# Optimization experiments

Measured on AMD Instinct MI355X. Metric: run time of the kernel, lower is better.

## Reference

```python
import jax, jax.numpy as jnp
import numpy as np

LN_EPS = 1e-3  # keras LayerNormalization default epsilon
H = 32


def _glorot(key, shape):
    fan_in, fan_out = shape[0], shape[1]
    lim = np.sqrt(6.0 / (fan_in + fan_out)).astype(np.float32)
    return jax.random.uniform(key, shape, jnp.float32, -lim, lim)


def setup_inputs() -> dict:
    key = jax.random.key(0)
    ks = jax.random.split(key, 10)
    ns, nc, d = 4096, 1024, 64
    num_seq, seq_len = 32, 256
    return {
        "sites": jax.random.normal(ks[0], (ns, d), jnp.float32),
        "cons": jax.random.normal(ks[1], (nc, d), jnp.float32),
        "idx_lower": jax.random.randint(ks[2], (ns,), 0, num_seq * seq_len, jnp.int32),
        "idx_higher": jax.random.randint(ks[3], (ns,), 0, num_seq * seq_len, jnp.int32),
        "W_s": _glorot(ks[4], (d, H)), "b_s": jnp.zeros((H,), jnp.float32),
        "W_c": _glorot(ks[5], (d, H)), "b_c": jnp.zeros((H,), jnp.float32),
        "W_d": _glorot(ks[6], (H, H)), "b_d": jnp.zeros((H,), jnp.float32),
        "ln_g": jnp.ones((H,), jnp.float32), "ln_b": jnp.zeros((H,), jnp.float32),
        "W_o": _glorot(ks[7], (H, 1)), "b_o": jnp.zeros((1,), jnp.float32),
        "num_seq": num_seq, "seq_len": seq_len,
    }


def reference(sites, cons, idx_lower, idx_higher, W_s, b_s, W_c, b_c,
              W_d, b_d, ln_g, ln_b, W_o, b_o, num_seq, seq_len):
    s = jax.nn.relu(sites @ W_s + b_s)          # [ns, 32]
    c = jax.nn.relu(cons @ W_c + b_c)           # [nc, 32]
    comb = s[:, None, :] + c[None, :, :]        # [ns, nc, 32] broadcast-sum
    h = comb @ W_d + b_d                        # decoder MLP: Dense(32)
    mu = jnp.mean(h, axis=-1, keepdims=True)
    var = jnp.var(h, axis=-1, keepdims=True)
    h = (h - mu) * jax.lax.rsqrt(var + LN_EPS) * ln_g + ln_b  # LayerNorm
    logits = (h @ W_o + b_o)[..., 0]            # [ns, nc]
    M = jax.nn.softmax(logits, axis=-1)

    nc_ = M.shape[1]
    slots = num_seq * seq_len

    def band(cum, idx):
        # scatter_nd (duplicate indices accumulate) onto slot grid
        Z = jnp.zeros((slots, nc_), M.dtype).at[idx].add(cum)
        Z = Z.reshape(num_seq, seq_len, nc_)
        p = jax.nn.relu(1.0 - Z)
        # exclusive cumprod along the position (seq_len) axis
        excl = jnp.cumprod(
            jnp.concatenate([jnp.ones_like(p[:, :1]), p[:, :-1]], axis=1), axis=1)
        return excl.reshape(slots, nc_)[idx]    # gather back per site

    M_c_lower = jnp.flip(jnp.cumsum(jnp.flip(M, -1), axis=-1), -1)  # reverse cumsum
    M_c_higher = jnp.cumsum(M, axis=-1)
    M_lower = band(M_c_lower, idx_lower)
    M_higher = band(M_c_higher, idx_higher)
    return M * M_lower * M_higher
```

## Files before the change

kernel.cpp:

```cpp
#include <hip/hip_runtime.h>

#define NS 4096
#define NCC 1024
#define DD 64
#define HH2 32
#define NSEQ 32
#define SLEN 256
#define SLOTS 8192
#define LNEPS 1e-3f
#define MAXSPS 1024

__global__ void __launch_bounds__(1024) k_setup(
    const float* __restrict__ sites, const float* __restrict__ cons,
    const float* __restrict__ Ws, const float* __restrict__ bs,
    const float* __restrict__ Wc, const float* __restrict__ bc,
    const float* __restrict__ Wd, const float* __restrict__ bd,
    const float* __restrict__ g, const float* __restrict__ Wo,
    float* __restrict__ u, float* __restrict__ A, float* __restrict__ P,
    float* __restrict__ v, float* __restrict__ B, float* __restrict__ Q,
    const int* __restrict__ idxl, const int* __restrict__ idxh,
    int* __restrict__ offl, int* __restrict__ slotl, int* __restrict__ sitel,
    int* __restrict__ offh, int* __restrict__ sloth, int* __restrict__ siteh) {
  __shared__ int cnt[SLOTS];
  __shared__ int wsumI[16];
  int tid = threadIdx.x;
  if (blockIdx.x < 5) {
    int t = blockIdx.x * 1024 + tid;
    if (t >= NS + NCC) return;
    bool isSite = t < NS;
    int row = isSite ? t : t - NS;
    const float* x = isSite ? sites + row * DD : cons + row * DD;
    const float* W1 = isSite ? Ws : Wc;
    const float* b1 = isSite ? bs : bc;
    float s[HH2];
#pragma unroll
    for (int h = 0; h < HH2; h++) s[h] = b1[h];
    for (int k = 0; k < DD; k++) {
      float xv = x[k];
#pragma unroll
      for (int h = 0; h < HH2; h++) s[h] = fmaf(xv, W1[k * HH2 + h], s[h]);
    }
#pragma unroll
    for (int h = 0; h < HH2; h++) s[h] = fmaxf(s[h], 0.0f);
    float hs[HH2];
#pragma unroll
    for (int h = 0; h < HH2; h++) hs[h] = isSite ? 0.0f : bd[h];
    for (int k = 0; k < HH2; k++) {
      float sv = s[k];
#pragma unroll
      for (int h = 0; h < HH2; h++) hs[h] = fmaf(sv, Wd[k * HH2 + h], hs[h]);
    }
    float mu = 0.f;
#pragma unroll
    for (int h = 0; h < HH2; h++) mu += hs[h];
    mu *= (1.0f / HH2);
    float p = 0.f, a = 0.f;
    float* dst = isSite ? (u + row * HH2) : (v + row * HH2);
#pragma unroll
    for (int h = 0; h < HH2; h++) {
      float uu = hs[h] - mu;
      dst[h] = uu;
      p += uu * uu;
      a = fmaf(uu * g[h], Wo[h], a);
    }
    p *= (1.0f / HH2);
    if (isSite) { A[row] = a; P[row] = p; } else { B[row] = a; Q[row] = p; }
    return;
  }
  int lane = tid & 63, wv = tid >> 6;
  int pass = blockIdx.x - 5;
  const int* idx = pass ? idxh : idxl;
  int* off = pass ? offh : offl;
  int* slotA = pass ? sloth : slotl;
  int* siteA = pass ? siteh : sitel;
  for (int i2 = tid; i2 < SLOTS; i2 += 1024) cnt[i2] = 0;
  __syncthreads();
  for (int i2 = tid; i2 < NS; i2 += 1024) atomicAdd(&cnt[idx[i2]], 1);
  __syncthreads();
  int base = tid * 8;
  int loc[8]; int sum = 0;
#pragma unroll
  for (int q2 = 0; q2 < 8; q2++) { loc[q2] = sum; sum += cnt[base + q2]; }
  int incl = sum;
#pragma unroll
  for (int o = 1; o < 64; o <<= 1) { int t2 = __shfl_up(incl, o); if (lane >= o) incl += t2; }
  if (lane == 63) wsumI[wv] = incl;
  __syncthreads();
  int wprev = 0;
#pragma unroll
  for (int w = 0; w < 16; w++) { int t3 = wsumI[w]; if (w < wv) wprev += t3; }
  int excl = wprev + (incl - sum);
  __syncthreads();
#pragma unroll
  for (int q2 = 0; q2 < 8; q2++) { int o2 = excl + loc[q2]; off[base + q2] = o2; cnt[base + q2] = o2; }
  if (tid == 0) off[SLOTS] = NS;
  __syncthreads();
  for (int i2 = tid; i2 < NS; i2 += 1024) {
    int sl = idx[i2];
    int pos = atomicAdd(&cnt[sl], 1);
    slotA[pos] = sl; siteA[pos] = i2;
  }
}

__global__ void __launch_bounds__(1024) k_main(const float* __restrict__ u,
    const float* __restrict__ A, const float* __restrict__ P,
    const float* __restrict__ v, const float* __restrict__ B, const float* __restrict__ Q,
    const float* __restrict__ lnb, const float* __restrict__ Wo, const float* __restrict__ bo,
    float* __restrict__ M, float* __restrict__ CLp, float* __restrict__ CHp) {
  int j = threadIdx.x;
  int lane = j & 63, wv = j >> 6;
  __shared__ float redA[16 * 16];
  __shared__ float redB[16 * 16];
  float4 vv[8];
  const float4* vp = (const float4*)(v + j * HH2);
#pragma unroll
  for (int q = 0; q < 8; q++) vv[q] = vp[q];
  float Bj = B[j], Qj = Q[j];
  float C = bo[0];
#pragma unroll
  for (int k = 0; k < HH2; k++) C = fmaf(lnb[k], Wo[k], C);
  int row0 = blockIdx.x * 16;

  float logit[16];
#pragma unroll
  for (int rr = 0; rr < 16; rr++) {
    int i = row0 + rr;
    const float4* up = (const float4*)(u + i * HH2);
    float dot = 0.f;
#pragma unroll
    for (int q = 0; q < 8; q++) {
      float4 u4 = up[q];
      dot = fmaf(u4.x, vv[q].x, dot);
      dot = fmaf(u4.y, vv[q].y, dot);
      dot = fmaf(u4.z, vv[q].z, dot);
      dot = fmaf(u4.w, vv[q].w, dot);
    }
    float var = P[i] + Qj + dot * 0.0625f;
    float lg = rsqrtf(var + LNEPS) * (A[i] + Bj) + C;
    logit[rr] = lg;
    float mx = lg;
#pragma unroll
    for (int o = 32; o > 0; o >>= 1) mx = fmaxf(mx, __shfl_xor(mx, o));
    if (lane == 0) redA[rr * 16 + wv] = mx;
  }
  __syncthreads();
  float e[16], incl[16];
#pragma unroll
  for (int rr = 0; rr < 16; rr++) {
    const float4* ra = (const float4*)(redA + rr * 16);
    float4 a0 = ra[0], a1 = ra[1], a2 = ra[2], a3 = ra[3];
    float mx = fmaxf(fmaxf(fmaxf(a0.x, a0.y), fmaxf(a0.z, a0.w)),
                     fmaxf(fmaxf(a1.x, a1.y), fmaxf(a1.z, a1.w)));
    mx = fmaxf(mx, fmaxf(fmaxf(fmaxf(a2.x, a2.y), fmaxf(a2.z, a2.w)),
                         fmaxf(fmaxf(a3.x, a3.y), fmaxf(a3.z, a3.w))));
    float ee = __expf(logit[rr] - mx);
    float ic = ee;
#pragma unroll
    for (int o = 1; o < 64; o <<= 1) { float tt = __shfl_up(ic, o); if (lane >= o) ic += tt; }
    if (lane == 63) redB[rr * 16 + wv] = ic;
    e[rr] = ee; incl[rr] = ic;
  }
  __syncthreads();
#pragma unroll
  for (int rr = 0; rr < 16; rr++) {
    const float4* rb = (const float4*)(redB + rr * 16);
    float4 b0 = rb[0], b1 = rb[1], b2 = rb[2], b3 = rb[3];
    float w_[16] = {b0.x, b0.y, b0.z, b0.w, b1.x, b1.y, b1.z, b1.w,
                    b2.x, b2.y, b2.z, b2.w, b3.x, b3.y, b3.z, b3.w};
    float prev = 0.f, tot = 0.f;
#pragma unroll
    for (int w = 0; w < 16; w++) { tot += w_[w]; if (w < wv) prev += w_[w]; }
    float chE = prev + incl[rr];
    float rd = 1.0f / tot;
    int o_ = (row0 + rr) * NCC + j;
    M[o_] = e[rr] * rd;
    CHp[o_] = chE * rd;
    CLp[o_] = (tot - chE + e[rr]) * rd;
  }
}

__global__ void __launch_bounds__(64, 1) k_band(const float* __restrict__ CLp, const float* __restrict__ CHp,
    const int* __restrict__ offl, const int* __restrict__ slotl, const int* __restrict__ sitel,
    const int* __restrict__ offh, const int* __restrict__ sloth, const int* __restrict__ siteh,
    float* __restrict__ EL, float* __restrict__ EH) {
  int band = blockIdx.z;
  const float* cum = band ? CHp : CLp;
  const int* off   = band ? offh : offl;
  const int* slotA = band ? sloth : slotl;
  const int* siteA = band ? siteh : sitel;
  float* E = band ? EH : EL;
  int seq = blockIdx.y;
  int j0 = blockIdx.x * 256 + threadIdx.x * 4;
  int s0 = off[seq * SLEN];
  int s1 = off[seq * SLEN + SLEN];
  int n = s1 - s0;

  __shared__ int s_site[MAXSPS];
  __shared__ int s_slot[MAXSPS];
  for (int i = threadIdx.x; i < n; i += 64) {
    s_site[i] = siteA[s0 + i];
    s_slot[i] = slotA[s0 + i];
  }
  __syncthreads();
  if (n <= 0) return;

  const int T = 8;
  float4 bufA[T], bufB[T];
#pragma unroll
  for (int k = 0; k < T; k++) {
    int kk = k < n ? k : n - 1;
    bufA[k] = *(const float4*)(cum + (size_t)s_site[kk] * NCC + j0);
  }
#pragma unroll
  for (int k = 0; k < T; k++) {
    int kk = T + k < n ? T + k : n - 1;
    bufB[k] = *(const float4*)(cum + (size_t)s_site[kk] * NCC + j0);
  }

  float4 r = make_float4(1.f, 1.f, 1.f, 1.f);
  float4 z = make_float4(0.f, 0.f, 0.f, 0.f);
  int prev = -1;
  int ntiles = (n + T - 1) / T;
  for (int t = 0; t < ntiles; t += 2) {
#pragma unroll
    for (int k = 0; k < T; k++) {
      int cur = t * T + k;
      if (cur < n) {
        float4 cv = bufA[k];
        int slot = s_slot[cur];
        if (slot != prev) {
          if (prev >= 0) {
            r.x *= fmaxf(1.f - z.x, 0.f);
            r.y *= fmaxf(1.f - z.y, 0.f);
            r.z *= fmaxf(1.f - z.z, 0.f);
            r.w *= fmaxf(1.f - z.w, 0.f);
            z = make_float4(0.f, 0.f, 0.f, 0.f);
          }
          prev = slot;
        }
        *(float4*)(E + (size_t)s_site[cur] * NCC + j0) = r;
        z.x += cv.x; z.y += cv.y; z.z += cv.z; z.w += cv.w;
      }
    }
#pragma unroll
    for (int k = 0; k < T; k++) {
      int idx2 = (t + 2) * T + k;
      int kk = idx2 < n ? idx2 : n - 1;
      bufA[k] = *(const float4*)(cum + (size_t)s_site[kk] * NCC + j0);
    }
#pragma unroll
    for (int k = 0; k < T; k++) {
      int cur = (t + 1) * T + k;
      if (cur < n) {
        float4 cv = bufB[k];
        int slot = s_slot[cur];
        if (slot != prev) {
          if (prev >= 0) {
            r.x *= fmaxf(1.f - z.x, 0.f);
            r.y *= fmaxf(1.f - z.y, 0.f);
            r.z *= fmaxf(1.f - z.z, 0.f);
            r.w *= fmaxf(1.f - z.w, 0.f);
            z = make_float4(0.f, 0.f, 0.f, 0.f);
          }
          prev = slot;
        }
        *(float4*)(E + (size_t)s_site[cur] * NCC + j0) = r;
        z.x += cv.x; z.y += cv.y; z.z += cv.z; z.w += cv.w;
      }
    }
#pragma unroll
    for (int k = 0; k < T; k++) {
      int idx2 = (t + 3) * T + k;
      int kk = idx2 < n ? idx2 : n - 1;
      bufB[k] = *(const float4*)(cum + (size_t)s_site[kk] * NCC + j0);
    }
  }
}

__global__ void k_final(float* __restrict__ out, const float* __restrict__ EL,
                        const float* __restrict__ EH) {
  int t = blockIdx.x * blockDim.x + threadIdx.x;
  float4 m = ((const float4*)out)[t];
  float4 a = ((const float4*)EL)[t];
  float4 b = ((const float4*)EH)[t];
  m.x *= a.x * b.x; m.y *= a.y * b.y; m.z *= a.z * b.z; m.w *= a.w * b.w;
  ((float4*)out)[t] = m;
}

extern "C" void kernel_launch(void* const* d_in, const int* in_sizes, int n_in,
                              void* d_out, int out_size, void* d_ws, size_t ws_size,
                              hipStream_t stream) {
  const float* sites = (const float*)d_in[0];
  const float* cons  = (const float*)d_in[1];
  const int* idxl = (const int*)d_in[2];
  const int* idxh = (const int*)d_in[3];
  const float* Ws = (const float*)d_in[4];
  const float* bs = (const float*)d_in[5];
  const float* Wc = (const float*)d_in[6];
  const float* bc = (const float*)d_in[7];
  const float* Wd = (const float*)d_in[8];
  const float* bd = (const float*)d_in[9];
  const float* lng = (const float*)d_in[10];
  const float* lnb = (const float*)d_in[11];
  const float* Wo = (const float*)d_in[12];
  const float* bo = (const float*)d_in[13];

  char* wsb = (char*)d_ws;
  size_t o = 0;
  auto alloc = [&](size_t bytes) { char* p = wsb + o; o += (bytes + 15) & ~(size_t)15; return p; };
  float* u   = (float*)alloc((size_t)NS * HH2 * 4);
  float* A   = (float*)alloc((size_t)NS * 4);
  float* P   = (float*)alloc((size_t)NS * 4);
  float* v   = (float*)alloc((size_t)NCC * HH2 * 4);
  float* B   = (float*)alloc((size_t)NCC * 4);
  float* Q   = (float*)alloc((size_t)NCC * 4);
  float* CLp = (float*)alloc((size_t)NS * NCC * 4);
  float* CHp = (float*)alloc((size_t)NS * NCC * 4);
  float* EL  = (float*)alloc((size_t)NS * NCC * 4);
  float* EH  = (float*)alloc((size_t)NS * NCC * 4);
  int* offl  = (int*)alloc((SLOTS + 1) * 4);
  int* slotl = (int*)alloc(NS * 4);
  int* sitel = (int*)alloc(NS * 4);
  int* offh  = (int*)alloc((SLOTS + 1) * 4);
  int* sloth = (int*)alloc(NS * 4);
  int* siteh = (int*)alloc(NS * 4);

  k_setup<<<7, 1024, 0, stream>>>(sites, cons, Ws, bs, Wc, bc, Wd, bd, lng, Wo,
                                  u, A, P, v, B, Q,
                                  idxl, idxh, offl, slotl, sitel, offh, sloth, siteh);
  k_main<<<NS / 16, 1024, 0, stream>>>(u, A, P, v, B, Q, lnb, Wo, bo,
                                       (float*)d_out, CLp, CHp);
  k_band<<<dim3(4, NSEQ, 2), 64, 0, stream>>>(CLp, CHp, offl, slotl, sitel,
                                              offh, sloth, siteh, EL, EH);
  k_final<<<(NS * NCC / 4) / 256, 256, 0, stream>>>((float*)d_out, EL, EH);
}
```

Before: 182.2 us.

## Fuse all stages into one cooperative persistent kernel with grid syncs

Replaces the four separate launches (setup, main softmax/cumsum, band scan, final multiply) with a single cooperative kernel of 256 blocks that runs each stage in turn, separated by grid-wide syncs. The band stage now gives each 64-lane wave one scalar column strip, mapping 1024 jobs onto 4 waves per block, instead of float4 strips in 64-thread blocks. The setup MLP is spread over 244 blocks of 21 active threads. The aim is to remove launch gaps and to use more of the device in the band stage. In exchange it adds grid-sync overhead, leaves most threads idle during setup, and truncates the per-sequence site count at 512 (MAXSPS cut from 1024), which could give wrong results if that many sites fall in one sequence.

```diff
diff --git a/kernel.cpp b/kernel.cpp
--- a/kernel.cpp
+++ b/kernel.cpp
@@ -1,4 +1,7 @@
 #include <hip/hip_runtime.h>
+#include <hip/hip_cooperative_groups.h>
+
+namespace cg = cooperative_groups;
 
 #define NS 4096
 #define NCC 1024
@@ -8,329 +11,318 @@
 #define SLEN 256
 #define SLOTS 8192
 #define LNEPS 1e-3f
-#define MAXSPS 1024
-
-__global__ void __launch_bounds__(1024) k_setup(
-    const float* __restrict__ sites, const float* __restrict__ cons,
-    const float* __restrict__ Ws, const float* __restrict__ bs,
-    const float* __restrict__ Wc, const float* __restrict__ bc,
-    const float* __restrict__ Wd, const float* __restrict__ bd,
-    const float* __restrict__ g, const float* __restrict__ Wo,
-    float* __restrict__ u, float* __restrict__ A, float* __restrict__ P,
-    float* __restrict__ v, float* __restrict__ B, float* __restrict__ Q,
-    const int* __restrict__ idxl, const int* __restrict__ idxh,
-    int* __restrict__ offl, int* __restrict__ slotl, int* __restrict__ sitel,
-    int* __restrict__ offh, int* __restrict__ sloth, int* __restrict__ siteh) {
-  __shared__ int cnt[SLOTS];
-  __shared__ int wsumI[16];
-  int tid = threadIdx.x;
-  if (blockIdx.x < 5) {
-    int t = blockIdx.x * 1024 + tid;
-    if (t >= NS + NCC) return;
-    bool isSite = t < NS;
-    int row = isSite ? t : t - NS;
-    const float* x = isSite ? sites + row * DD : cons + row * DD;
-    const float* W1 = isSite ? Ws : Wc;
-    const float* b1 = isSite ? bs : bc;
-    float s[HH2];
-#pragma unroll
-    for (int h = 0; h < HH2; h++) s[h] = b1[h];
-    for (int k = 0; k < DD; k++) {
-      float xv = x[k];
-#pragma unroll
-      for (int h = 0; h < HH2; h++) s[h] = fmaf(xv, W1[k * HH2 + h], s[h]);
-    }
-#pragma unroll
-    for (int h = 0; h < HH2; h++) s[h] = fmaxf(s[h], 0.0f);
-    float hs[HH2];
-#pragma unroll
-    for (int h = 0; h < HH2; h++) hs[h] = isSite ? 0.0f : bd[h];
-    for (int k = 0; k < HH2; k++) {
-      float sv = s[k];
-#pragma unroll
-      for (int h = 0; h < HH2; h++) hs[h] = fmaf(sv, Wd[k * HH2 + h], hs[h]);
-    }
-    float mu = 0.f;
-#pragma unroll
-    for (int h = 0; h < HH2; h++) mu += hs[h];
-    mu *= (1.0f / HH2);
-    float p = 0.f, a = 0.f;
-    float* dst = isSite ? (u + row * HH2) : (v + row * HH2);
-#pragma unroll
-    for (int h = 0; h < HH2; h++) {
-      float uu = hs[h] - mu;
-      dst[h] = uu;
-      p += uu * uu;
-      a = fmaf(uu * g[h], Wo[h], a);
-    }
-    p *= (1.0f / HH2);
-    if (isSite) { A[row] = a; P[row] = p; } else { B[row] = a; Q[row] = p; }
-    return;
+#define MAXSPS 512
+
+struct Params {
+  const float *sites, *cons;
+  const int *idxl, *idxh;
+  const float *Ws, *bs, *Wc, *bc, *Wd, *bd, *lng, *lnb, *Wo, *bo;
+  float *out;
+  float *u, *A, *P, *v, *B, *Q, *CL, *CH, *EL, *EH;
+  int *offl, *slotl, *sitel, *offh, *sloth, *siteh;
+};
+
+__global__ void __launch_bounds__(1024, 4) k_all(Params p) {
+  __shared__ union SM {
+    struct { int cnt[SLOTS]; int wsum[16]; } sort;
+    struct { float redA[256]; float redB[256]; } red;
+    struct { int site[4][MAXSPS]; int slot[4][MAXSPS]; } band;
+  } sm;
+  cg::grid_group grid = cg::this_grid();
+  int b = blockIdx.x, tid = threadIdx.x;
+  int lane = tid & 63, wv = tid >> 6;
+
+  if (b < 2) {
+    const int* idx = b ? p.idxh : p.idxl;
+    int* off = b ? p.offh : p.offl;
+    int* slotA = b ? p.sloth : p.slotl;
+    int* siteA = b ? p.siteh : p.sitel;
+    for (int i2 = tid; i2 < SLOTS; i2 += 1024) sm.sort.cnt[i2] = 0;
+    __syncthreads();
+    for (int i2 = tid; i2 < NS; i2 += 1024) atomicAdd(&sm.sort.cnt[idx[i2]], 1);
+    __syncthreads();
+    int base = tid * 8;
+    int loc[8]; int sum = 0;
+#pragma unroll
+    for (int q2 = 0; q2 < 8; q2++) { loc[q2] = sum; sum += sm.sort.cnt[base + q2]; }
+    int incl = sum;
+#pragma unroll
+    for (int o = 1; o < 64; o <<= 1) { int t2 = __shfl_up(incl, o); if (lane >= o) incl += t2; }
+    if (lane == 63) sm.sort.wsum[wv] = incl;
+    __syncthreads();
+    int wprev = 0;
+#pragma unroll
+    for (int w = 0; w < 16; w++) { int t3 = sm.sort.wsum[w]; if (w < wv) wprev += t3; }
+    int excl = wprev + (incl - sum);
+    __syncthreads();
+#pragma unroll
+    for (int q2 = 0; q2 < 8; q2++) { int o2 = excl + loc[q2]; off[base + q2] = o2; sm.sort.cnt[base + q2] = o2; }
+    if (tid == 0) off[SLOTS] = NS;
+    __syncthreads();
+    for (int i2 = tid; i2 < NS; i2 += 1024) {
+      int sl = idx[i2];
+      int pos = atomicAdd(&sm.sort.cnt[sl], 1);
+      slotA[pos] = sl; siteA[pos] = i2;
+    }
+  } else if (b < 246 && tid < 21) {
+    int t = (b - 2) * 21 + tid;
+    if (t < NS + NCC) {
+      bool isSite = t < NS;
+      int row = isSite ? t : t - NS;
+      const float* x = isSite ? p.sites + row * DD : p.cons + row * DD;
+      const float* W1 = isSite ? p.Ws : p.Wc;
+      const float* b1 = isSite ? p.bs : p.bc;
+      float s[HH2];
+#pragma unroll
+      for (int h = 0; h < HH2; h++) s[h] = b1[h];
+      for (int k = 0; k < DD; k++) {
+        float xv = x[k];
+#pragma unroll
+        for (int h = 0; h < HH2; h++) s[h] = fmaf(xv, W1[k * HH2 + h], s[h]);
+      }
+#pragma unroll
+      for (int h = 0; h < HH2; h++) s[h] = fmaxf(s[h], 0.0f);
+      float hs[HH2];
+#pragma unroll
+      for (int h = 0; h < HH2; h++) hs[h] = isSite ? 0.0f : p.bd[h];
+      for (int k = 0; k < HH2; k++) {
+        float sv = s[k];
+#pragma unroll
+        for (int h = 0; h < HH2; h++) hs[h] = fmaf(sv, p.Wd[k * HH2 + h], hs[h]);
+      }
+      float mu = 0.f;
+#pragma unroll
+      for (int h = 0; h < HH2; h++) mu += hs[h];
+      mu *= (1.0f / HH2);
+      float pp = 0.f, a = 0.f;
+      float* dst = isSite ? (p.u + row * HH2) : (p.v + row * HH2);
+#pragma unroll
+      for (int h = 0; h < HH2; h++) {
+        float uu = hs[h] - mu;
+        dst[h] = uu;
+        pp += uu * uu;
+        a = fmaf(uu * p.lng[h], p.Wo[h], a);
+      }
+      pp *= (1.0f / HH2);
+      if (isSite) { p.A[row] = a; p.P[row] = pp; } else { p.B[row] = a; p.Q[row] = pp; }
+    }
   }
-  int lane = tid & 63, wv = tid >> 6;
-  int pass = blockIdx.x - 5;
-  const int* idx = pass ? idxh : idxl;
-  int* off = pass ? offh : offl;
-  int* slotA = pass ? sloth : slotl;
-  int* siteA = pass ? siteh : sitel;
-  for (int i2 = tid; i2 < SLOTS; i2 += 1024) cnt[i2] = 0;
-  __syncthreads();
-  for (int i2 = tid; i2 < NS; i2 += 1024) atomicAdd(&cnt[idx[i2]], 1);
-  __syncthreads();
-  int base = tid * 8;
-  int loc[8]; int sum = 0;
-#pragma unroll
-  for (int q2 = 0; q2 < 8; q2++) { loc[q2] = sum; sum += cnt[base + q2]; }
-  int incl = sum;
-#pragma unroll
-  for (int o = 1; o < 64; o <<= 1) { int t2 = __shfl_up(incl, o); if (lane >= o) incl += t2; }
-  if (lane == 63) wsumI[wv] = incl;
-  __syncthreads();
-  int wprev = 0;
-#pragma unroll
-  for (int w = 0; w < 16; w++) { int t3 = wsumI[w]; if (w < wv) wprev += t3; }
-  int excl = wprev + (incl - sum);
-  __syncthreads();
-#pragma unroll
-  for (int q2 = 0; q2 < 8; q2++) { int o2 = excl + loc[q2]; off[base + q2] = o2; cnt[base + q2] = o2; }
-  if (tid == 0) off[SLOTS] = NS;
-  __syncthreads();
-  for (int i2 = tid; i2 < NS; i2 += 1024) {
-    int sl = idx[i2];
-    int pos = atomicAdd(&cnt[sl], 1);
-    slotA[pos] = sl; siteA[pos] = i2;
+  __threadfence();
+  grid.sync();
+
+  {
+    int j = tid;
+    float4 vv[8];
+    const float4* vp = (const float4*)(p.v + j * HH2);
+#pragma unroll
+    for (int q = 0; q < 8; q++) vv[q] = vp[q];
+    float Bj = p.B[j], Qj = p.Q[j];
+    float C = p.bo[0];
+#pragma unroll
+    for (int k = 0; k < HH2; k++) C = fmaf(p.lnb[k], p.Wo[k], C);
+    int row0 = b * 16;
+
+    float logit[16];
+#pragma unroll
+    for (int rr = 0; rr < 16; rr++) {
+      int i = row0 + rr;
+      const float4* up = (const float4*)(p.u + i * HH2);
+      float dot = 0.f;
+#pragma unroll
+      for (int q = 0; q < 8; q++) {
+        float4 u4 = up[q];
+        dot = fmaf(u4.x, vv[q].x, dot);
+        dot = fmaf(u4.y, vv[q].y, dot);
+        dot = fmaf(u4.z, vv[q].z, dot);
+        dot = fmaf(u4.w, vv[q].w, dot);
+      }
+      float var = p.P[i] + Qj + dot * 0.0625f;
+      float lg = rsqrtf(var + LNEPS) * (p.A[i] + Bj) + C;
+      logit[rr] = lg;
+      float mx = lg;
+#pragma unroll
+      for (int o = 32; o > 0; o >>= 1) mx = fmaxf(mx, __shfl_xor(mx, o));
+      if (lane == 0) sm.red.redA[rr * 16 + wv] = mx;
+    }
+    __syncthreads();
+    float e[16], incl[16];
+#pragma unroll
+    for (int rr = 0; rr < 16; rr++) {
+      const float4* ra = (const float4*)(sm.red.redA + rr * 16);
+      float4 a0 = ra[0], a1 = ra[1], a2 = ra[2], a3 = ra[3];
+      float mx = fmaxf(fmaxf(fmaxf(a0.x, a0.y), fmaxf(a0.z, a0.w)),
+                       fmaxf(fmaxf(a1.x, a1.y), fmaxf(a1.z, a1.w)));
+      mx = fmaxf(mx, fmaxf(fmaxf(fmaxf(a2.x, a2.y), fmaxf(a2.z, a2.w)),
+                           fmaxf(fmaxf(a3.x, a3.y), fmaxf(a3.z, a3.w))));
+      float ee = __expf(logit[rr] - mx);
+      float ic = ee;
+#pragma unroll
+      for (int o = 1; o < 64; o <<= 1) { float tt = __shfl_up(ic, o); if (lane >= o) ic += tt; }
+      if (lane == 63) sm.red.redB[rr * 16 + wv] = ic;
+      e[rr] = ee; incl[rr] = ic;
+    }
+    __syncthreads();
+#pragma unroll
+    for (int rr = 0; rr < 16; rr++) {
+      const float4* rb = (const float4*)(sm.red.redB + rr * 16);
+      float4 b0 = rb[0], b1 = rb[1], b2 = rb[2], b3 = rb[3];
+      float w_[16] = {b0.x, b0.y, b0.z, b0.w, b1.x, b1.y, b1.z, b1.w,
+                      b2.x, b2.y, b2.z, b2.w, b3.x, b3.y, b3.z, b3.w};
+      float prev = 0.f, tot = 0.f;
+#pragma unroll
+      for (int w = 0; w < 16; w++) { tot += w_[w]; if (w < wv) prev += w_[w]; }
+      float chE = prev + incl[rr];
+      float rd = 1.0f / tot;
+      int o_ = (row0 + rr) * NCC + j;
+      p.out[o_] = e[rr] * rd;
+      p.CH[o_] = chE * rd;
+      p.CL[o_] = (tot - chE + e[rr]) * rd;
+    }
   }
-}
-
-__global__ void __launch_bounds__(1024) k_main(const float* __restrict__ u,
-    const float* __restrict__ A, const float* __restrict__ P,
-    const float* __restrict__ v, const float* __restrict__ B, const float* __restrict__ Q,
-    const float* __restrict__ lnb, const float* __restrict__ Wo, const float* __restrict__ bo,
-    float* __restrict__ M, float* __restrict__ CLp, float* __restrict__ CHp) {
-  int j = threadIdx.x;
-  int lane = j & 63, wv = j >> 6;
-  __shared__ float redA[16 * 16];
-  __shared__ float redB[16 * 16];
-  float4 vv[8];
-  const float4* vp = (const float4*)(v + j * HH2);
-#pragma unroll
-  for (int q = 0; q < 8; q++) vv[q] = vp[q];
-  float Bj = B[j], Qj = Q[j];
-  float C = bo[0];
-#pragma unroll
-  for (int k = 0; k < HH2; k++) C = fmaf(lnb[k], Wo[k], C);
-  int row0 = blockIdx.x * 16;
-
-  float logit[16];
-#pragma unroll
-  for (int rr = 0; rr < 16; rr++) {
-    int i = row0 + rr;
-    const float4* up = (const float4*)(u + i * HH2);
-    float dot = 0.f;
-#pragma unroll
-    for (int q = 0; q < 8; q++) {
-      float4 u4 = up[q];
-      dot = fmaf(u4.x, vv[q].x, dot);
-      dot = fmaf(u4.y, vv[q].y, dot);
-      dot = fmaf(u4.z, vv[q].z, dot);
-      dot = fmaf(u4.w, vv[q].w, dot);
-    }
-    float var = P[i] + Qj + dot * 0.0625f;
-    float lg = rsqrtf(var + LNEPS) * (A[i] + Bj) + C;
-    logit[rr] = lg;
-    float mx = lg;
-#pragma unroll
-    for (int o = 32; o > 0; o >>= 1) mx = fmaxf(mx, __shfl_xor(mx, o));
-    if (lane == 0) redA[rr * 16 + wv] = mx;
+  __threadfence();
+  grid.sync();
+
+  if (wv < 4) {
+    int job = wv * 256 + b;
+    int band = job >> 9;
+    int rem = job & 511;
+    int seq = rem >> 4;
+    int ct = rem & 15;
+    const float* cum = band ? p.CH : p.CL;
+    const int* off = band ? p.offh : p.offl;
+    const int* slotA = band ? p.sloth : p.slotl;
+    const int* siteA = band ? p.siteh : p.sitel;
+    float* E = band ? p.EH : p.EL;
+    int j = ct * 64 + lane;
+    int s0 = off[seq * SLEN];
+    int s1 = off[seq * SLEN + SLEN];
+    int n = s1 - s0;
+    if (n > MAXSPS) n = MAXSPS;
+    int* ss = sm.band.site[wv];
+    int* sl = sm.band.slot[wv];
+    for (int i = lane; i < n; i += 64) {
+      ss[i] = siteA[s0 + i];
+      sl[i] = slotA[s0 + i];
+    }
+    __asm__ __volatile__("s_waitcnt lgkmcnt(0)" ::: "memory");
+    if (n > 0) {
+      const int T = 8;
+      float bufA[T], bufB[T];
+#pragma unroll
+      for (int k = 0; k < T; k++) {
+        int kk = k < n ? k : n - 1;
+        bufA[k] = cum[(size_t)ss[kk] * NCC + j];
+      }
+#pragma unroll
+      for (int k = 0; k < T; k++) {
+        int kk = T + k < n ? T + k : n - 1;
+        bufB[k] = cum[(size_t)ss[kk] * NCC + j];
+      }
+      float r = 1.f, z = 0.f;
+      int prev = -1;
+      int ntiles = (n + T - 1) / T;
+      for (int t = 0; t < ntiles; t += 2) {
+#pragma unroll
+        for (int k = 0; k < T; k++) {
+          int cur = t * T + k;
+          if (cur < n) {
+            float cv = bufA[k];
+            int slot = sl[cur];
+            if (slot != prev) {
+              if (prev >= 0) { r *= fmaxf(1.f - z, 0.f); z = 0.f; }
+              prev = slot;
+            }
+            E[(size_t)ss[cur] * NCC + j] = r;
+            z += cv;
+          }
+        }
+#pragma unroll
+        for (int k = 0; k < T; k++) {
+          int idx2 = (t + 2) * T + k;
+          int kk = idx2 < n ? idx2 : n - 1;
+          bufA[k] = cum[(size_t)ss[kk] * NCC + j];
+        }
+#pragma unroll
+        for (int k = 0; k < T; k++) {
+          int cur = (t + 1) * T + k;
+          if (cur < n) {
+            float cv = bufB[k];
+            int slot = sl[cur];
+            if (slot != prev) {
+              if (prev >= 0) { r *= fmaxf(1.f - z, 0.f); z = 0.f; }
+              prev = slot;
+            }
+            E[(size_t)ss[cur] * NCC + j] = r;
+            z += cv;
+          }
+        }
+#pragma unroll
+        for (int k = 0; k < T; k++) {
+          int idx2 = (t + 3) * T + k;
+          int kk = idx2 < n ? idx2 : n - 1;
+          bufB[k] = cum[(size_t)ss[kk] * NCC + j];
+        }
+      }
+    }
   }
-  __syncthreads();
-  float e[16], incl[16];
-#pragma unroll
-  for (int rr = 0; rr < 16; rr++) {
-    const float4* ra = (const float4*)(redA + rr * 16);
-    float4 a0 = ra[0], a1 = ra[1], a2 = ra[2], a3 = ra[3];
-    float mx = fmaxf(fmaxf(fmaxf(a0.x, a0.y), fmaxf(a0.z, a0.w)),
-                     fmaxf(fmaxf(a1.x, a1.y), fmaxf(a1.z, a1.w)));
-    mx = fmaxf(mx, fmaxf(fmaxf(fmaxf(a2.x, a2.y), fmaxf(a2.z, a2.w)),
-                         fmaxf(fmaxf(a3.x, a3.y), fmaxf(a3.z, a3.w))));
-    float ee = __expf(logit[rr] - mx);
-    float ic = ee;
-#pragma unroll
-    for (int o = 1; o < 64; o <<= 1) { float tt = __shfl_up(ic, o); if (lane >= o) ic += tt; }
-    if (lane == 63) redB[rr * 16 + wv] = ic;
-    e[rr] = ee; incl[rr] = ic;
+  __threadfence();
+  grid.sync();
+
+  {
+    float4* o4 = (float4*)p.out;
+    const float4* a4 = (const float4*)p.EL;
+    const float4* b4 = (const float4*)p.EH;
+    const int total = NS * NCC / 4;
+    for (int i = b * 1024 + tid; i < total; i += 256 * 1024) {
+      float4 m = o4[i];
+      float4 a = a4[i];
+      float4 bb = b4[i];
+      m.x *= a.x * bb.x; m.y *= a.y * bb.y; m.z *= a.z * bb.z; m.w *= a.w * bb.w;
+      o4[i] = m;
+    }
   }
-  __syncthreads();
-#pragma unroll
-  for (int rr = 0; rr < 16; rr++) {
-    const float4* rb = (const float4*)(redB + rr * 16);
-    float4 b0 = rb[0], b1 = rb[1], b2 = rb[2], b3 = rb[3];
-    float w_[16] = {b0.x, b0.y, b0.z, b0.w, b1.x, b1.y, b1.z, b1.w,
-                    b2.x, b2.y, b2.z, b2.w, b3.x, b3.y, b3.z, b3.w};
-    float prev = 0.f, tot = 0.f;
-#pragma unroll
-    for (int w = 0; w < 16; w++) { tot += w_[w]; if (w < wv) prev += w_[w]; }
-    float chE = prev + incl[rr];
-    float rd = 1.0f / tot;
-    int o_ = (row0 + rr) * NCC + j;
-    M[o_] = e[rr] * rd;
-    CHp[o_] = chE * rd;
-    CLp[o_] = (tot - chE + e[rr]) * rd;
-  }
-}
-
-__global__ void __launch_bounds__(64, 1) k_band(const float* __restrict__ CLp, const float* __restrict__ CHp,
-    const int* __restrict__ offl, const int* __restrict__ slotl, const int* __restrict__ sitel,
-    const int* __restrict__ offh, const int* __restrict__ sloth, const int* __restrict__ siteh,
-    float* __restrict__ EL, float* __restrict__ EH) {
-  int band = blockIdx.z;
-  const float* cum = band ? CHp : CLp;
-  const int* off   = band ? offh : offl;
-  const int* slotA = band ? sloth : slotl;
-  const int* siteA = band ? siteh : sitel;
-  float* E = band ? EH : EL;
-  int seq = blockIdx.y;
-  int j0 = blockIdx.x * 256 + threadIdx.x * 4;
-  int s0 = off[seq * SLEN];
-  int s1 = off[seq * SLEN + SLEN];
-  int n = s1 - s0;
-
-  __shared__ int s_site[MAXSPS];
-  __shared__ int s_slot[MAXSPS];
-  for (int i = threadIdx.x; i < n; i += 64) {
-    s_site[i] = siteA[s0 + i];
-    s_slot[i] = slotA[s0 + i];
-  }
-  __syncthreads();
-  if (n <= 0) return;
-
-  const int T = 8;
-  float4 bufA[T], bufB[T];
-#pragma unroll
-  for (int k = 0; k < T; k++) {
-    int kk = k < n ? k : n - 1;
-    bufA[k] = *(const float4*)(cum + (size_t)s_site[kk] * NCC + j0);
-  }
-#pragma unroll
-  for (int k = 0; k < T; k++) {
-    int kk = T + k < n ? T + k : n - 1;
-    bufB[k] = *(const float4*)(cum + (size_t)s_site[kk] * NCC + j0);
-  }
-
-  float4 r = make_float4(1.f, 1.f, 1.f, 1.f);
-  float4 z = make_float4(0.f, 0.f, 0.f, 0.f);
-  int prev = -1;
-  int ntiles = (n + T - 1) / T;
-  for (int t = 0; t < ntiles; t += 2) {
-#pragma unroll
-    for (int k = 0; k < T; k++) {
-      int cur = t * T + k;
-      if (cur < n) {
-        float4 cv = bufA[k];
-        int slot = s_slot[cur];
-        if (slot != prev) {
-          if (prev >= 0) {
-            r.x *= fmaxf(1.f - z.x, 0.f);
-            r.y *= fmaxf(1.f - z.y, 0.f);
-            r.z *= fmaxf(1.f - z.z, 0.f);
-            r.w *= fmaxf(1.f - z.w, 0.f);
-            z = make_float4(0.f, 0.f, 0.f, 0.f);
-          }
-          prev = slot;
-        }
-        *(float4*)(E + (size_t)s_site[cur] * NCC + j0) = r;
-        z.x += cv.x; z.y += cv.y; z.z += cv.z; z.w += cv.w;
-      }
-    }
-#pragma unroll
-    for (int k = 0; k < T; k++) {
-      int idx2 = (t + 2) * T + k;
-      int kk = idx2 < n ? idx2 : n - 1;
-      bufA[k] = *(const float4*)(cum + (size_t)s_site[kk] * NCC + j0);
-    }
-#pragma unroll
-    for (int k = 0; k < T; k++) {
-      int cur = (t + 1) * T + k;
-      if (cur < n) {
-        float4 cv = bufB[k];
-        int slot = s_slot[cur];
-        if (slot != prev) {
-          if (prev >= 0) {
-            r.x *= fmaxf(1.f - z.x, 0.f);
-            r.y *= fmaxf(1.f - z.y, 0.f);
-            r.z *= fmaxf(1.f - z.z, 0.f);
-            r.w *= fmaxf(1.f - z.w, 0.f);
-            z = make_float4(0.f, 0.f, 0.f, 0.f);
-          }
-          prev = slot;
-        }
-        *(float4*)(E + (size_t)s_site[cur] * NCC + j0) = r;
-        z.x += cv.x; z.y += cv.y; z.z += cv.z; z.w += cv.w;
-      }
-    }
-#pragma unroll
-    for (int k = 0; k < T; k++) {
-      int idx2 = (t + 3) * T + k;
-      int kk = idx2 < n ? idx2 : n - 1;
-      bufB[k] = *(const float4*)(cum + (size_t)s_site[kk] * NCC + j0);
-    }
-  }
-}
-
-__global__ void k_final(float* __restrict__ out, const float* __restrict__ EL,
-                        const float* __restrict__ EH) {
-  int t = blockIdx.x * blockDim.x + threadIdx.x;
-  float4 m = ((const float4*)out)[t];
-  float4 a = ((const float4*)EL)[t];
-  float4 b = ((const float4*)EH)[t];
-  m.x *= a.x * b.x; m.y *= a.y * b.y; m.z *= a.z * b.z; m.w *= a.w * b.w;
-  ((float4*)out)[t] = m;
 }
 
 extern "C" void kernel_launch(void* const* d_in, const int* in_sizes, int n_in,
                               void* d_out, int out_size, void* d_ws, size_t ws_size,
                               hipStream_t stream) {
-  const float* sites = (const float*)d_in[0];
-  const float* cons  = (const float*)d_in[1];
-  const int* idxl = (const int*)d_in[2];
-  const int* idxh = (const int*)d_in[3];
-  const float* Ws = (const float*)d_in[4];
-  const float* bs = (const float*)d_in[5];
-  const float* Wc = (const float*)d_in[6];
-  const float* bc = (const float*)d_in[7];
-  const float* Wd = (const float*)d_in[8];
-  const float* bd = (const float*)d_in[9];
-  const float* lng = (const float*)d_in[10];
-  const float* lnb = (const float*)d_in[11];
-  const float* Wo = (const float*)d_in[12];
-  const float* bo = (const float*)d_in[13];
-
   char* wsb = (char*)d_ws;
   size_t o = 0;
-  auto alloc = [&](size_t bytes) { char* p = wsb + o; o += (bytes + 15) & ~(size_t)15; return p; };
-  float* u   = (float*)alloc((size_t)NS * HH2 * 4);
-  float* A   = (float*)alloc((size_t)NS * 4);
-  float* P   = (float*)alloc((size_t)NS * 4);
-  float* v   = (float*)alloc((size_t)NCC * HH2 * 4);
-  float* B   = (float*)alloc((size_t)NCC * 4);
-  float* Q   = (float*)alloc((size_t)NCC * 4);
-  float* CLp = (float*)alloc((size_t)NS * NCC * 4);
-  float* CHp = (float*)alloc((size_t)NS * NCC * 4);
-  float* EL  = (float*)alloc((size_t)NS * NCC * 4);
-  float* EH  = (float*)alloc((size_t)NS * NCC * 4);
-  int* offl  = (int*)alloc((SLOTS + 1) * 4);
-  int* slotl = (int*)alloc(NS * 4);
-  int* sitel = (int*)alloc(NS * 4);
-  int* offh  = (int*)alloc((SLOTS + 1) * 4);
-  int* sloth = (int*)alloc(NS * 4);
-  int* siteh = (int*)alloc(NS * 4);
-
-  k_setup<<<7, 1024, 0, stream>>>(sites, cons, Ws, bs, Wc, bc, Wd, bd, lng, Wo,
-                                  u, A, P, v, B, Q,
-                                  idxl, idxh, offl, slotl, sitel, offh, sloth, siteh);
-  k_main<<<NS / 16, 1024, 0, stream>>>(u, A, P, v, B, Q, lnb, Wo, bo,
-                                       (float*)d_out, CLp, CHp);
-  k_band<<<dim3(4, NSEQ, 2), 64, 0, stream>>>(CLp, CHp, offl, slotl, sitel,
-                                              offh, sloth, siteh, EL, EH);
-  k_final<<<(NS * NCC / 4) / 256, 256, 0, stream>>>((float*)d_out, EL, EH);
+  auto alloc = [&](size_t bytes) { char* pz = wsb + o; o += (bytes + 15) & ~(size_t)15; return pz; };
+
+  Params pr;
+  pr.sites = (const float*)d_in[0];
+  pr.cons  = (const float*)d_in[1];
+  pr.idxl  = (const int*)d_in[2];
+  pr.idxh  = (const int*)d_in[3];
+  pr.Ws = (const float*)d_in[4];
+  pr.bs = (const float*)d_in[5];
+  pr.Wc = (const float*)d_in[6];
+  pr.bc = (const float*)d_in[7];
+  pr.Wd = (const float*)d_in[8];
+  pr.bd = (const float*)d_in[9];
+  pr.lng = (const float*)d_in[10];
+  pr.lnb = (const float*)d_in[11];
+  pr.Wo = (const float*)d_in[12];
+  pr.bo = (const float*)d_in[13];
+  pr.out = (float*)d_out;
+  pr.u = (float*)alloc((size_t)NS * HH2 * 4);
+  pr.A = (float*)alloc((size_t)NS * 4);
+  pr.P = (float*)alloc((size_t)NS * 4);
+  pr.v = (float*)alloc((size_t)NCC * HH2 * 4);
+  pr.B = (float*)alloc((size_t)NCC * 4);
+  pr.Q = (float*)alloc((size_t)NCC * 4);
+  pr.CL = (float*)alloc((size_t)NS * NCC * 4);
+  pr.CH = (float*)alloc((size_t)NS * NCC * 4);
+  pr.EL = (float*)alloc((size_t)NS * NCC * 4);
+  pr.EH = (float*)alloc((size_t)NS * NCC * 4);
+  pr.offl = (int*)alloc((SLOTS + 1) * 4);
+  pr.slotl = (int*)alloc(NS * 4);
+  pr.sitel = (int*)alloc(NS * 4);
+  pr.offh = (int*)alloc((SLOTS + 1) * 4);
+  pr.sloth = (int*)alloc(NS * 4);
+  pr.siteh = (int*)alloc(NS * 4);
+
+  void* kp[] = { &pr };
+  hipLaunchCooperativeKernel((const void*)k_all, dim3(256), dim3(1024), kp, 0, stream);
 }
```

New measurement: 563.2 us. 3.09x slower.

## Split band kernel per side, fuse final product into high band pass

Applied to the files above, without the earlier changes.

The combined band kernel is split into separate low and high passes. Each pass now runs twice as many blocks by having every thread handle float2 instead of float4. The high pass reads M and EL and writes the final output directly, which removes the EH buffer and the separate elementwise k_final kernel along with their full-size reads and writes. The setup kernel's projection part is spread over 20 blocks of 256 active threads to use more CUs. The cost is two serialized band launches, each with only 256 blocks of 64 threads, and more live registers in the high pass.

```diff
diff --git a/kernel.cpp b/kernel.cpp
--- a/kernel.cpp
+++ b/kernel.cpp
@@ -24,8 +24,9 @@
   __shared__ int cnt[SLOTS];
   __shared__ int wsumI[16];
   int tid = threadIdx.x;
-  if (blockIdx.x < 5) {
-    int t = blockIdx.x * 1024 + tid;
+  if (blockIdx.x < 20) {
+    if (tid >= 256) return;
+    int t = blockIdx.x * 256 + tid;
     if (t >= NS + NCC) return;
     bool isSite = t < NS;
     int row = isSite ? t : t - NS;
@@ -68,7 +69,7 @@
     return;
   }
   int lane = tid & 63, wv = tid >> 6;
-  int pass = blockIdx.x - 5;
+  int pass = blockIdx.x - 20;
   const int* idx = pass ? idxh : idxl;
   int* off = pass ? offh : offl;
   int* slotA = pass ? sloth : slotl;
@@ -179,46 +180,34 @@
   }
 }
 
-__global__ void __launch_bounds__(64, 1) k_band(const float* __restrict__ CLp, const float* __restrict__ CHp,
+__global__ void __launch_bounds__(64, 1) k_bandL(const float* __restrict__ CLp,
     const int* __restrict__ offl, const int* __restrict__ slotl, const int* __restrict__ sitel,
-    const int* __restrict__ offh, const int* __restrict__ sloth, const int* __restrict__ siteh,
-    float* __restrict__ EL, float* __restrict__ EH) {
-  int band = blockIdx.z;
-  const float* cum = band ? CHp : CLp;
-  const int* off   = band ? offh : offl;
-  const int* slotA = band ? sloth : slotl;
-  const int* siteA = band ? siteh : sitel;
-  float* E = band ? EH : EL;
+    float* __restrict__ EL) {
   int seq = blockIdx.y;
-  int j0 = blockIdx.x * 256 + threadIdx.x * 4;
-  int s0 = off[seq * SLEN];
-  int s1 = off[seq * SLEN + SLEN];
+  int j0 = blockIdx.x * 128 + threadIdx.x * 2;
+  int s0 = offl[seq * SLEN];
+  int s1 = offl[seq * SLEN + SLEN];
   int n = s1 - s0;
-
-  __shared__ int s_site[MAXSPS];
-  __shared__ int s_slot[MAXSPS];
-  for (int i = threadIdx.x; i < n; i += 64) {
-    s_site[i] = siteA[s0 + i];
-    s_slot[i] = slotA[s0 + i];
-  }
+  __shared__ int ss[MAXSPS];
+  __shared__ int sl[MAXSPS];
+  for (int i = threadIdx.x; i < n; i += 64) { ss[i] = sitel[s0 + i]; sl[i] = slotl[s0 + i]; }
   __syncthreads();
   if (n <= 0) return;
 
   const int T = 8;
-  float4 bufA[T], bufB[T];
+  float2 bufA[T], bufB[T];
 #pragma unroll
   for (int k = 0; k < T; k++) {
     int kk = k < n ? k : n - 1;
-    bufA[k] = *(const float4*)(cum + (size_t)s_site[kk] * NCC + j0);
+    bufA[k] = *(const float2*)(CLp + (size_t)ss[kk] * NCC + j0);
   }
 #pragma unroll
   for (int k = 0; k < T; k++) {
     int kk = T + k < n ? T + k : n - 1;
-    bufB[k] = *(const float4*)(cum + (size_t)s_site[kk] * NCC + j0);
-  }
-
-  float4 r = make_float4(1.f, 1.f, 1.f, 1.f);
-  float4 z = make_float4(0.f, 0.f, 0.f, 0.f);
+    bufB[k] = *(const float2*)(CLp + (size_t)ss[kk] * NCC + j0);
+  }
+  float2 r = make_float2(1.f, 1.f);
+  float2 z = make_float2(0.f, 0.f);
   int prev = -1;
   int ntiles = (n + T - 1) / T;
   for (int t = 0; t < ntiles; t += 2) {
@@ -226,65 +215,151 @@
     for (int k = 0; k < T; k++) {
       int cur = t * T + k;
       if (cur < n) {
-        float4 cv = bufA[k];
-        int slot = s_slot[cur];
+        float2 cv = bufA[k];
+        int slot = sl[cur];
         if (slot != prev) {
           if (prev >= 0) {
             r.x *= fmaxf(1.f - z.x, 0.f);
             r.y *= fmaxf(1.f - z.y, 0.f);
-            r.z *= fmaxf(1.f - z.z, 0.f);
-            r.w *= fmaxf(1.f - z.w, 0.f);
-            z = make_float4(0.f, 0.f, 0.f, 0.f);
+            z = make_float2(0.f, 0.f);
           }
           prev = slot;
         }
-        *(float4*)(E + (size_t)s_site[cur] * NCC + j0) = r;
-        z.x += cv.x; z.y += cv.y; z.z += cv.z; z.w += cv.w;
+        *(float2*)(EL + (size_t)ss[cur] * NCC + j0) = r;
+        z.x += cv.x; z.y += cv.y;
       }
     }
 #pragma unroll
     for (int k = 0; k < T; k++) {
       int idx2 = (t + 2) * T + k;
       int kk = idx2 < n ? idx2 : n - 1;
-      bufA[k] = *(const float4*)(cum + (size_t)s_site[kk] * NCC + j0);
+      bufA[k] = *(const float2*)(CLp + (size_t)ss[kk] * NCC + j0);
     }
 #pragma unroll
     for (int k = 0; k < T; k++) {
       int cur = (t + 1) * T + k;
       if (cur < n) {
-        float4 cv = bufB[k];
-        int slot = s_slot[cur];
+        float2 cv = bufB[k];
+        int slot = sl[cur];
         if (slot != prev) {
           if (prev >= 0) {
             r.x *= fmaxf(1.f - z.x, 0.f);
             r.y *= fmaxf(1.f - z.y, 0.f);
-            r.z *= fmaxf(1.f - z.z, 0.f);
-            r.w *= fmaxf(1.f - z.w, 0.f);
-            z = make_float4(0.f, 0.f, 0.f, 0.f);
+            z = make_float2(0.f, 0.f);
           }
           prev = slot;
         }
-        *(float4*)(E + (size_t)s_site[cur] * NCC + j0) = r;
-        z.x += cv.x; z.y += cv.y; z.z += cv.z; z.w += cv.w;
+        *(float2*)(EL + (size_t)ss[cur] * NCC + j0) = r;
+        z.x += cv.x; z.y += cv.y;
       }
     }
 #pragma unroll
     for (int k = 0; k < T; k++) {
       int idx2 = (t + 3) * T + k;
       int kk = idx2 < n ? idx2 : n - 1;
-      bufB[k] = *(const float4*)(cum + (size_t)s_site[kk] * NCC + j0);
+      bufB[k] = *(const float2*)(CLp + (size_t)ss[kk] * NCC + j0);
     }
   }
 }
 
-__global__ void k_final(float* __restrict__ out, const float* __restrict__ EL,
-                        const float* __restrict__ EH) {
-  int t = blockIdx.x * blockDim.x + threadIdx.x;
-  float4 m = ((const float4*)out)[t];
-  float4 a = ((const float4*)EL)[t];
-  float4 b = ((const float4*)EH)[t];
-  m.x *= a.x * b.x; m.y *= a.y * b.y; m.z *= a.z * b.z; m.w *= a.w * b.w;
-  ((float4*)out)[t] = m;
+__global__ void __launch_bounds__(64, 1) k_bandH(const float* __restrict__ CHp,
+    const int* __restrict__ offh, const int* __restrict__ sloth, const int* __restrict__ siteh,
+    const float* __restrict__ EL, float* __restrict__ out) {
+  int seq = blockIdx.y;
+  int j0 = blockIdx.x * 128 + threadIdx.x * 2;
+  int s0 = offh[seq * SLEN];
+  int s1 = offh[seq * SLEN + SLEN];
+  int n = s1 - s0;
+  __shared__ int ss[MAXSPS];
+  __shared__ int sl[MAXSPS];
+  for (int i = threadIdx.x; i < n; i += 64) { ss[i] = siteh[s0 + i]; sl[i] = sloth[s0 + i]; }
+  __syncthreads();
+  if (n <= 0) return;
+
+  const int T = 8;
+  float2 cA[T], cB[T], mA[T], mB[T], eA[T], eB[T];
+#pragma unroll
+  for (int k = 0; k < T; k++) {
+    int kk = k < n ? k : n - 1;
+    size_t base = (size_t)ss[kk] * NCC + j0;
+    cA[k] = *(const float2*)(CHp + base);
+    mA[k] = *(const float2*)(out + base);
+    eA[k] = *(const float2*)(EL + base);
+  }
+#pragma unroll
+  for (int k = 0; k < T; k++) {
+    int kk = T + k < n ? T + k : n - 1;
+    size_t base = (size_t)ss[kk] * NCC + j0;
+    cB[k] = *(const float2*)(CHp + base);
+    mB[k] = *(const float2*)(out + base);
+    eB[k] = *(const float2*)(EL + base);
+  }
+  float2 r = make_float2(1.f, 1.f);
+  float2 z = make_float2(0.f, 0.f);
+  int prev = -1;
+  int ntiles = (n + T - 1) / T;
+  for (int t = 0; t < ntiles; t += 2) {
+#pragma unroll
+    for (int k = 0; k < T; k++) {
+      int cur = t * T + k;
+      if (cur < n) {
+        float2 cv = cA[k], mv = mA[k], ev = eA[k];
+        int slot = sl[cur];
+        if (slot != prev) {
+          if (prev >= 0) {
+            r.x *= fmaxf(1.f - z.x, 0.f);
+            r.y *= fmaxf(1.f - z.y, 0.f);
+            z = make_float2(0.f, 0.f);
+          }
+          prev = slot;
+        }
+        float2 ov;
+        ov.x = mv.x * ev.x * r.x;
+        ov.y = mv.y * ev.y * r.y;
+        *(float2*)(out + (size_t)ss[cur] * NCC + j0) = ov;
+        z.x += cv.x; z.y += cv.y;
+      }
+    }
+#pragma unroll
+    for (int k = 0; k < T; k++) {
+      int idx2 = (t + 2) * T + k;
+      int kk = idx2 < n ? idx2 : n - 1;
+      size_t base = (size_t)ss[kk] * NCC + j0;
+      cA[k] = *(const float2*)(CHp + base);
+      mA[k] = *(const float2*)(out + base);
+      eA[k] = *(const float2*)(EL + base);
+    }
+#pragma unroll
+    for (int k = 0; k < T; k++) {
+      int cur = (t + 1) * T + k;
+      if (cur < n) {
+        float2 cv = cB[k], mv = mB[k], ev = eB[k];
+        int slot = sl[cur];
+        if (slot != prev) {
+          if (prev >= 0) {
+            r.x *= fmaxf(1.f - z.x, 0.f);
+            r.y *= fmaxf(1.f - z.y, 0.f);
+            z = make_float2(0.f, 0.f);
+          }
+          prev = slot;
+        }
+        float2 ov;
+        ov.x = mv.x * ev.x * r.x;
+        ov.y = mv.y * ev.y * r.y;
+        *(float2*)(out + (size_t)ss[cur] * NCC + j0) = ov;
+        z.x += cv.x; z.y += cv.y;
+      }
+    }
+#pragma unroll
+    for (int k = 0; k < T; k++) {
+      int idx2 = (t + 3) * T + k;
+      int kk = idx2 < n ? idx2 : n - 1;
+      size_t base = (size_t)ss[kk] * NCC + j0;
+      cB[k] = *(const float2*)(CHp + base);
+      mB[k] = *(const float2*)(out + base);
+      eB[k] = *(const float2*)(EL + base);
+    }
+  }
 }
 
 extern "C" void kernel_launch(void* const* d_in, const int* in_sizes, int n_in,
@@ -317,7 +392,6 @@
   float* CLp = (float*)alloc((size_t)NS * NCC * 4);
   float* CHp = (float*)alloc((size_t)NS * NCC * 4);
   float* EL  = (float*)alloc((size_t)NS * NCC * 4);
-  float* EH  = (float*)alloc((size_t)NS * NCC * 4);
   int* offl  = (int*)alloc((SLOTS + 1) * 4);
   int* slotl = (int*)alloc(NS * 4);
   int* sitel = (int*)alloc(NS * 4);
@@ -325,12 +399,11 @@
   int* sloth = (int*)alloc(NS * 4);
   int* siteh = (int*)alloc(NS * 4);
 
-  k_setup<<<7, 1024, 0, stream>>>(sites, cons, Ws, bs, Wc, bc, Wd, bd, lng, Wo,
-                                  u, A, P, v, B, Q,
-                                  idxl, idxh, offl, slotl, sitel, offh, sloth, siteh);
+  k_setup<<<22, 1024, 0, stream>>>(sites, cons, Ws, bs, Wc, bc, Wd, bd, lng, Wo,
+                                   u, A, P, v, B, Q,
+                                   idxl, idxh, offl, slotl, sitel, offh, sloth, siteh);
   k_main<<<NS / 16, 1024, 0, stream>>>(u, A, P, v, B, Q, lnb, Wo, bo,
                                        (float*)d_out, CLp, CHp);
-  k_band<<<dim3(4, NSEQ, 2), 64, 0, stream>>>(CLp, CHp, offl, slotl, sitel,
-                                              offh, sloth, siteh, EL, EH);
-  k_final<<<(NS * NCC / 4) / 256, 256, 0, stream>>>((float*)d_out, EL, EH);
+  k_bandL<<<dim3(8, NSEQ), 64, 0, stream>>>(CLp, offl, slotl, sitel, EL);
+  k_bandH<<<dim3(8, NSEQ), 64, 0, stream>>>(CHp, offh, sloth, siteh, EL, (float*)d_out);
 }
```

Result: no change. 185.6 us (+1.9%).
